# Performance work log

Hardware: AMD Instinct MI355X
Metric: run time of the kernel (lower is better)

## Reference

```python
import jax, jax.numpy as jnp
import numpy as np

B, DIM, N = 64, 128, 4000
H = 4
DH = DIM // H          # 32
CL = 50                # clusters (hardcoded in module)
K = 9                  # knn_num
SCALOR = DH ** -0.5


def setup_inputs() -> dict:
    key = jax.random.key(0)
    ks = jax.random.split(key, 16)
    s = 0.05
    inp = {
        'x': jax.random.normal(ks[0], (B, DIM, N, 1), jnp.float32),
        # conv_group1 / conv_group2: InstanceNorm(no affine) -> BN(affine) -> ReLU -> 1x1 conv
        'wg1': jax.random.normal(ks[1], (CL, DIM), jnp.float32) * s,
        'bg1': jnp.zeros((CL,), jnp.float32),
        'g1_gamma': jnp.ones((DIM,), jnp.float32),
        'g1_beta': jnp.zeros((DIM,), jnp.float32),
        'wg2': jax.random.normal(ks[2], (CL, DIM), jnp.float32) * s,
        'bg2': jnp.zeros((CL,), jnp.float32),
        'g2_gamma': jnp.ones((DIM,), jnp.float32),
        'g2_beta': jnp.zeros((DIM,), jnp.float32),
        # per-head 1x1 convs (stacked over heads)
        'qkv_w': jax.random.normal(ks[3], (H, DH, DIM), jnp.float32) * s,
        'qkv_b': jnp.zeros((H, DH), jnp.float32),
        'qkv1_w': jax.random.normal(ks[4], (H, 3 * DH, DIM), jnp.float32) * s,
        'qkv1_b': jnp.zeros((H, 3 * DH), jnp.float32),
        # GCBlock convs: conv1 (1,3) stride (1,3): 2*DH->DH ; conv2 (1,3): DH->DH
        'gc1_w': jax.random.normal(ks[5], (H, DH, 2 * DH, 3), jnp.float32) * s,
        'gc1_b': jnp.zeros((H, DH), jnp.float32),
        'gc1_gamma': jnp.ones((H, DH), jnp.float32),
        'gc1_beta': jnp.zeros((H, DH), jnp.float32),
        'gc2_w': jax.random.normal(ks[6], (H, DH, DH, 3), jnp.float32) * s,
        'gc2_b': jnp.zeros((H, DH), jnp.float32),
        'gc2_gamma': jnp.ones((H, DH), jnp.float32),
        'gc2_beta': jnp.zeros((H, DH), jnp.float32),
        # output projections
        'pres_w': jax.random.normal(ks[7], (DIM, 2 * DIM), jnp.float32) * s,
        'pres_b': jnp.zeros((DIM,), jnp.float32),
        'proj_w': jax.random.normal(ks[8], (DIM, DIM), jnp.float32) * s,
        'proj_b': jnp.zeros((DIM,), jnp.float32),
    }
    return inp


def _conv_group(x3, w, bconv, gamma, beta):
    # x3: (b, C, n). InstanceNorm2d(eps=1e-3, no affine) over n, BN(train) over (b,n), ReLU, 1x1 conv.
    mu = x3.mean(-1, keepdims=True)
    var = x3.var(-1, keepdims=True)
    xin = (x3 - mu) * jax.lax.rsqrt(var + 1e-3)
    mu2 = xin.mean((0, 2), keepdims=True)
    var2 = xin.var((0, 2), keepdims=True)
    xbn = gamma[None, :, None] * (xin - mu2) * jax.lax.rsqrt(var2 + 1e-5) + beta[None, :, None]
    xr = jax.nn.relu(xbn)
    return jnp.einsum('oc,bcn->bon', w, xr) + bconv[None, :, None]


def _bn_train(h, gamma, beta, axes):
    mu = h.mean(axes, keepdims=True)
    var = h.var(axes, keepdims=True)
    return gamma * (h - mu) * jax.lax.rsqrt(var + 1e-5) + beta


def _forward(x, wg1, bg1, g1_gamma, g1_beta, wg2, bg2, g2_gamma, g2_beta,
             qkv_w, qkv_b, qkv1_w, qkv1_b,
             gc1_w, gc1_b, gc1_gamma, gc1_beta,
             gc2_w, gc2_b, gc2_gamma, gc2_beta,
             pres_w, pres_b, proj_w, proj_b):
    xs = x[..., 0]                                          # (b, dim, n)
    # cluster assignment 1: softmax over points
    embed1 = _conv_group(xs, wg1, bg1, g1_gamma, g1_beta)   # (b, 50, n)
    S1 = jax.nn.softmax(embed1, axis=2)
    cluster_x = jnp.einsum('bdn,bcn->bdc', xs, S1)          # (b, dim, 50)

    # ---- local branch (per head, vectorized): 1x1 conv -> knn graph feature -> conv stack ----
    q = jnp.einsum('hod,bdc->bhoc', qkv_w, cluster_x) + qkv_b[None, :, :, None]  # (b,H,dh,50)
    xt = q.transpose(0, 1, 3, 2)                            # (b,H,50,dh)
    inner = jnp.einsum('bhnc,bhmc->bhnm', xt, xt)
    sq = jnp.sum(xt * xt, axis=-1)
    pd = 2.0 * inner - sq[..., :, None] - sq[..., None, :]  # negative squared distance
    idx = jax.lax.top_k(pd, K)[1]                            # (b,H,50,K)
    x_exp = jnp.broadcast_to(xt[:, :, None, :, :], xt.shape[:2] + (CL, CL, DH))
    feature = jnp.take_along_axis(x_exp, idx[..., None], axis=3)        # (b,H,50,K,dh)
    center = jnp.broadcast_to(xt[:, :, :, None, :], feature.shape)
    edge = jnp.concatenate([center, center - feature], axis=-1)          # (b,H,50,K,2dh)
    # conv1: kernel (1,3) stride (1,3): K=9 -> 3 windows of 3
    e = edge.reshape(edge.shape[0], H, CL, 3, 3, 2 * DH)
    h1 = jnp.einsum('bhnjti,hoit->bhnjo', e, gc1_w) + gc1_b[None, :, None, None, :]
    h1 = jax.nn.relu(_bn_train(h1, gc1_gamma[None, :, None, None, :], gc1_beta[None, :, None, None, :], (0, 2, 3)))
    # conv2: kernel (1,3): 3 -> 1
    h2 = jnp.einsum('bhnti,hoit->bhno', h1, gc2_w) + gc2_b[None, :, None, :]
    h2 = jax.nn.relu(_bn_train(h2, gc2_gamma[None, :, None, :], gc2_beta[None, :, None, :], (0, 2)))
    local = h2.transpose(0, 1, 3, 2)                        # (b,H,dh,50)

    # ---- global branch: tiny attention over 50 clusters per head ----
    qkv = jnp.einsum('hod,bdc->bhoc', qkv1_w, cluster_x) + qkv1_b[None, :, :, None]  # (b,H,3dh,50)
    qg, kg, vg = jnp.split(qkv, 3, axis=2)
    attn = jax.nn.softmax(SCALOR * jnp.einsum('bhdn,bhdm->bhnm', qg, kg), axis=-1)
    glob = jnp.einsum('bhnm,bhdm->bhdn', attn, vg)          # (b,H,dh,50)

    # interleave [local_h, global_h] per head along channels -> (b, 2*dim, 50)
    per_head = jnp.concatenate([local, glob], axis=2)       # (b,H,2dh,50)
    cat = per_head.reshape(per_head.shape[0], 2 * DIM, CL)
    res = jnp.einsum('oc,bcn->bon', pres_w, cat) + pres_b[None, :, None]  # (b,dim,50)

    # cluster assignment 2: softmax over clusters, scatter back to points
    embed2 = _conv_group(xs, wg2, bg2, g2_gamma, g2_beta)   # (b,50,n)
    S2 = jax.nn.softmax(embed2, axis=1)
    res2 = jnp.einsum('bdc,bcn->bdn', res, S2)              # (b,dim,n)
    out = jnp.einsum('od,bdn->bon', proj_w, res2) + proj_b[None, :, None]
    return out[..., None]                                   # (b,dim,n,1)


def reference(x, wg1, bg1, g1_gamma, g1_beta, wg2, bg2, g2_gamma, g2_beta,
              qkv_w, qkv_b, qkv1_w, qkv1_b,
              gc1_w, gc1_b, gc1_gamma, gc1_beta,
              gc2_w, gc2_b, gc2_gamma, gc2_beta,
              pres_w, pres_b, proj_w, proj_b):
    return _forward(x, wg1, bg1, g1_gamma, g1_beta, wg2, bg2, g2_gamma, g2_beta,
                    qkv_w, qkv_b, qkv1_w, qkv1_b,
                    gc1_w, gc1_b, gc1_gamma, gc1_beta,
                    gc2_w, gc2_b, gc2_gamma, gc2_beta,
                    pres_w, pres_b, proj_w, proj_b)
```

## Files before the change

kernel.cpp:

```cpp
#include <hip/hip_runtime.h>
#include <cstddef>


constexpr size_t O_MU    = 0;
constexpr size_t O_RINV  = 8192;
constexpr size_t O_RATIO = 16384;
constexpr size_t O_A1    = 24576;
constexpr size_t O_B1    = 24704;
constexpr size_t O_A2    = 24832;
constexpr size_t O_B2    = 24960;
constexpr size_t O_PROJWT= 25088;
constexpr size_t O_VPROJ = 41472;
constexpr size_t O_MT    = 41600;
constexpr size_t O_E2    = 74368;
constexpr size_t O_UCXP  = 12874368;
constexpr size_t O_W1T   = 18551424;
constexpr size_t O_W2T   = 18558080;
constexpr size_t O_XT    = 18564736;
constexpr size_t O_QT    = 18974336;
constexpr size_t O_KT    = 19383936;
constexpr size_t O_VT    = 19793536;
constexpr size_t O_H1    = 20203136;
constexpr size_t O_P1    = 21431936;
constexpr size_t O_H2    = 21448320;
constexpr size_t O_P2    = 21857920;
constexpr size_t O_CAT   = 21874240;
constexpr size_t O_PRES2 = 22693440;

__global__ __launch_bounds__(256) void k_stats(const float* __restrict__ x,
                                               const float* __restrict__ projw,
                                               const float* __restrict__ wg1,
                                               const float* __restrict__ wg2,
                                               float* __restrict__ ws){
  if(blockIdx.x >= 2112){
    const float* src = (blockIdx.x == 2112) ? wg1 : wg2;
    size_t dst = (blockIdx.x == 2112) ? O_W1T : O_W2T;
    for(int i = threadIdx.x; i < 6656; i += 256){
      int c = i / 52, cl = i % 52;
      ws[dst + i] = (cl < 50) ? src[cl*128 + c] : 0.f;
    }
    return;
  }
  if(blockIdx.x >= 2048){
    int i = (blockIdx.x - 2048)*256 + threadIdx.x;
    int o = i & 127, k = i >> 7;
    ws[O_PROJWT + i] = projw[o*128 + k];
    return;
  }
  int w = threadIdx.x >> 6, lane = threadIdx.x & 63;
  int row = blockIdx.x*4 + w;
  const float4* xr = (const float4*)(x + (size_t)row * 4000);
  float s = 0.f, sq = 0.f;
  for(int i = lane; i < 1000; i += 64){
    float4 v = xr[i];
    s  += v.x + v.y + v.z + v.w;
    sq += v.x*v.x + v.y*v.y + v.z*v.z + v.w*v.w;
  }
  for(int off = 32; off > 0; off >>= 1){
    s  += __shfl_down(s,  off, 64);
    sq += __shfl_down(sq, off, 64);
  }
  if(lane == 0){
    float mean = s * (1.f/4000.f);
    float var  = sq * (1.f/4000.f) - mean*mean;
    ws[O_MU   + row] = mean;
    ws[O_RINV + row] = rsqrtf(var + 1e-3f);
    ws[O_RATIO+ row] = var / (var + 1e-3f);
  }
}

__global__ __launch_bounds__(256) void k_mprep(const float* __restrict__ presw,
                                               const float* __restrict__ presb,
                                               const float* __restrict__ g1g,
                                               const float* __restrict__ g1b,
                                               const float* __restrict__ g2g,
                                               const float* __restrict__ g2b,
                                               float* __restrict__ ws){
  int t = threadIdx.x;
  if(blockIdx.x < 128){
    int kk2 = blockIdx.x * 2;
    __shared__ float pwc[2][128];
    { int which = t >> 7, d = t & 127; pwc[which][d] = presw[d*256 + kk2 + which]; }
    __syncthreads();
    int which = t >> 7, o = t & 127;
    float acc = 0.f;
    for(int d = 0; d < 128; d++) acc += ws[O_PROJWT + d*128 + o] * pwc[which][d];
    ws[O_MT + (size_t)(kk2 + which)*128 + o] = acc;
  }else if(blockIdx.x == 128){
    if(t < 128){
      float v = 0.f;
      for(int d = 0; d < 128; d++) v += ws[O_PROJWT + d*128 + t] * presb[d];
      ws[O_VPROJ + t] = v;
    }
  }else{
    if(t < 128){
      float s = 0.f;
      for(int b = 0; b < 64; b++) s += ws[O_RATIO + b*128 + t];
      float var2 = s * (1.f/64.f);
      float inv2 = rsqrtf(var2 + 1e-5f);
      ws[O_A1+t] = g1g[t] * inv2;  ws[O_B1+t] = g1b[t];
      ws[O_A2+t] = g2g[t] * inv2;  ws[O_B2+t] = g2b[t];
    }
  }
}

__global__ __launch_bounds__(256, 3) void k_e1ucx(const float* __restrict__ x,
    const float* __restrict__ bg1, float* __restrict__ ws){
  int ch = blockIdx.x, b = blockIdx.y;
  __shared__ float lrv1[128*48];
  __shared__ float lxt [48*128];
  __shared__ float ca1[128], cb1[128];
  __shared__ float bg1p[56];
  int t = threadIdx.x;
  if(t < 128){
    float mu = ws[O_MU + b*128 + t], ri = ws[O_RINV + b*128 + t];
    float a1 = ws[O_A1+t]*ri;
    ca1[t] = a1; cb1[t] = ws[O_B1+t] - a1*mu;
  }
  if(t >= 192 && t < 248){ int q = t - 192; bg1p[q] = (q < 50) ? bg1[q] : 0.f; }
  const float* W1T = ws + O_W1T;
  int dg = t & 31, cg = t >> 5;
  int d4 = dg*4, c8 = cg*8;
  float ua[4][8];
  #pragma unroll
  for(int r = 0; r < 4; r++)
    #pragma unroll
    for(int i = 0; i < 8; i++) ua[r][i] = 0.f;
  float zacc = 0.f;
  int ig = t >> 4, jg = t & 15;
  int clb = ig*4, j4 = jg*4;
  int sc[6], sj[6], cx[6];
  float4 pf[6];
  #pragma unroll
  for(int j = 0; j < 6; j++){
    int i = t + 256*j;
    sc[j] = i/12; sj[j] = (i%12)*4;
    cx[j] = sc[j] ^ (((sj[j] >> 2) & 7) << 2);
  }
  {
    int nb0 = ch*336;
    int lim0 = 4000 - nb0; if(lim0 > 48) lim0 = 48;
    #pragma unroll
    for(int j = 0; j < 6; j++)
      pf[j] = (sj[j] < lim0) ? *(const float4*)&x[(size_t)(b*128 + sc[j])*4000 + nb0 + sj[j]]
                             : make_float4(0.f,0.f,0.f,0.f);
  }

  for(int st = 0; st < 7; st++){
    int lim = 4000 - (ch*336 + st*48); if(lim > 48) lim = 48;
    __syncthreads();
    #pragma unroll
    for(int j = 0; j < 6; j++){
      int c = sc[j], jj = sj[j], cxx = cx[j];
      float4 xv = (jj < lim) ? pf[j] : make_float4(0.f,0.f,0.f,0.f);
      lxt[(jj+0)*128 + cxx] = xv.x; lxt[(jj+1)*128 + cxx] = xv.y;
      lxt[(jj+2)*128 + cxx] = xv.z; lxt[(jj+3)*128 + cxx] = xv.w;
      float a1 = ca1[c], b1v = cb1[c];
      float4 r1;
      r1.x = fmaxf(a1*xv.x + b1v, 0.f); r1.y = fmaxf(a1*xv.y + b1v, 0.f);
      r1.z = fmaxf(a1*xv.z + b1v, 0.f); r1.w = fmaxf(a1*xv.w + b1v, 0.f);
      *(float4*)&lrv1[c*48 + jj] = r1;
    }
    __syncthreads();
    if(st < 6){
      int nb2 = ch*336 + (st+1)*48;
      int lim2 = 4000 - nb2; if(lim2 > 48) lim2 = 48;
      #pragma unroll
      for(int j = 0; j < 6; j++)
        pf[j] = (sj[j] < lim2) ? *(const float4*)&x[(size_t)(b*128 + sc[j])*4000 + nb2 + sj[j]]
                               : make_float4(0.f,0.f,0.f,0.f);
    }
    float e[4][4];
    if(ig < 13 && jg < 12){
      #pragma unroll
      for(int r = 0; r < 4; r++){ e[r][0]=0.f; e[r][1]=0.f; e[r][2]=0.f; e[r][3]=0.f; }
      #pragma unroll 4
      for(int c = 0; c < 128; c++){
        float4 w = *(const float4*)&W1T[c*52 + clb];
        float4 v = *(const float4*)&lrv1[c*48 + j4];
        e[0][0] += w.x*v.x; e[0][1] += w.x*v.y; e[0][2] += w.x*v.z; e[0][3] += w.x*v.w;
        e[1][0] += w.y*v.x; e[1][1] += w.y*v.y; e[1][2] += w.y*v.z; e[1][3] += w.y*v.w;
        e[2][0] += w.z*v.x; e[2][1] += w.z*v.y; e[2][2] += w.z*v.z; e[2][3] += w.z*v.w;
        e[3][0] += w.w*v.x; e[3][1] += w.w*v.y; e[3][2] += w.w*v.z; e[3][3] += w.w*v.w;
      }
    }
    __syncthreads();
    if(ig < 13 && jg < 12){
      bool live = (j4 < lim);
      #pragma unroll
      for(int r = 0; r < 4; r++){
        float bias = bg1p[clb + r];
        float4 u = make_float4(0.f,0.f,0.f,0.f);
        if(live){
          u.x = expf(e[r][0] + bias); u.y = expf(e[r][1] + bias);
          u.z = expf(e[r][2] + bias); u.w = expf(e[r][3] + bias);
        }
        *(float4*)&lrv1[(clb + r)*48 + j4] = u;
      }
    }
    __syncthreads();
    if(cg < 7){
      #pragma unroll 2
      for(int n4 = 0; n4 < 12; n4++){
        int n0 = n4*4;
        int dx = d4 ^ ((n4 & 7) << 2);
        float4 uv[8];
        #pragma unroll
        for(int i = 0; i < 8; i++) uv[i] = *(const float4*)&lrv1[(c8 + i)*48 + n0];
        float4 x0 = *(const float4*)&lxt[(n0+0)*128 + dx];
        float4 x1 = *(const float4*)&lxt[(n0+1)*128 + dx];
        float4 x2 = *(const float4*)&lxt[(n0+2)*128 + dx];
        float4 x3 = *(const float4*)&lxt[(n0+3)*128 + dx];
        #pragma unroll
        for(int i = 0; i < 8; i++){
          ua[0][i] += x0.x*uv[i].x + x1.x*uv[i].y + x2.x*uv[i].z + x3.x*uv[i].w;
          ua[1][i] += x0.y*uv[i].x + x1.y*uv[i].y + x2.y*uv[i].z + x3.y*uv[i].w;
          ua[2][i] += x0.z*uv[i].x + x1.z*uv[i].y + x2.z*uv[i].z + x3.z*uv[i].w;
          ua[3][i] += x0.w*uv[i].x + x1.w*uv[i].y + x2.w*uv[i].z + x3.w*uv[i].w;
        }
      }
    }
    if(t < 52){
      float s = 0.f;
      #pragma unroll
      for(int k = 0; k < 12; k++){
        float4 u = *(const float4*)&lrv1[t*48 + k*4];
        s += u.x + u.y + u.z + u.w;
      }
      zacc += s;
    }
  }
  if(cg < 7){
    #pragma unroll
    for(int r = 0; r < 4; r++){
      size_t base = O_UCXP + ((size_t)(ch*64 + b)*132 + d4 + r)*56 + c8;
      *(float4*)&ws[base]     = make_float4(ua[r][0], ua[r][1], ua[r][2], ua[r][3]);
      *(float4*)&ws[base + 4] = make_float4(ua[r][4], ua[r][5], ua[r][6], ua[r][7]);
    }
  }
  if(t < 52) ws[O_UCXP + ((size_t)(ch*64 + b)*132 + 128)*56 + t] = zacc;
}

__global__ __launch_bounds__(256, 6) void k_e2(const float* __restrict__ x,
    const float* __restrict__ bg2, float* __restrict__ ws){
  int ch = blockIdx.x, b = blockIdx.y;
  __shared__ float lrv2[128*48];
  __shared__ float ca2[128], cb2[128];
  __shared__ float bg2p[56];
  int t = threadIdx.x;
  if(t < 128){
    float mu = ws[O_MU + b*128 + t], ri = ws[O_RINV + b*128 + t];
    float a2 = ws[O_A2+t]*ri;
    ca2[t] = a2; cb2[t] = ws[O_B2+t] - a2*mu;
  }
  if(t >= 192 && t < 248){ int q = t - 192; bg2p[q] = (q < 50) ? bg2[q] : 0.f; }
  const float* W2T = ws + O_W2T;
  int ig = t >> 4, jg = t & 15;
  int clb = ig*4, j4 = jg*4;
  int sc[6], sj[6];
  float4 pf[6];
  #pragma unroll
  for(int j = 0; j < 6; j++){ int i = t + 256*j; sc[j] = i/12; sj[j] = (i%12)*4; }
  {
    int nb0 = ch*168;
    int lim0 = 4000 - nb0; if(lim0 > 48) lim0 = 48;
    #pragma unroll
    for(int j = 0; j < 6; j++)
      pf[j] = (sj[j] < lim0) ? *(const float4*)&x[(size_t)(b*128 + sc[j])*4000 + nb0 + sj[j]]
                             : make_float4(0.f,0.f,0.f,0.f);
  }
  for(int st = 0; st < 4; st++){
    int nb = ch*168 + st*48;
    int lim = 4000 - nb; if(lim > 48) lim = 48;
    __syncthreads();
    #pragma unroll
    for(int j = 0; j < 6; j++){
      int c = sc[j], jj = sj[j];
      float4 xv = (jj < lim) ? pf[j] : make_float4(0.f,0.f,0.f,0.f);
      float a2 = ca2[c], b2v = cb2[c];
      float4 r2;
      r2.x = fmaxf(a2*xv.x + b2v, 0.f); r2.y = fmaxf(a2*xv.y + b2v, 0.f);
      r2.z = fmaxf(a2*xv.z + b2v, 0.f); r2.w = fmaxf(a2*xv.w + b2v, 0.f);
      *(float4*)&lrv2[c*48 + jj] = r2;
    }
    __syncthreads();
    if(st < 3){
      int nb2 = nb + 48;
      int lim2 = 4000 - nb2; if(lim2 > 48) lim2 = 48;
      #pragma unroll
      for(int j = 0; j < 6; j++)
        pf[j] = (sj[j] < lim2) ? *(const float4*)&x[(size_t)(b*128 + sc[j])*4000 + nb2 + sj[j]]
                               : make_float4(0.f,0.f,0.f,0.f);
    }
    if(ig < 13 && jg < 12 && lim > 0){
      float e[4][4];
      #pragma unroll
      for(int r = 0; r < 4; r++){ e[r][0]=0.f; e[r][1]=0.f; e[r][2]=0.f; e[r][3]=0.f; }
      #pragma unroll 4
      for(int c = 0; c < 128; c++){
        float4 w = *(const float4*)&W2T[c*52 + clb];
        float4 v = *(const float4*)&lrv2[c*48 + j4];
        e[0][0] += w.x*v.x; e[0][1] += w.x*v.y; e[0][2] += w.x*v.z; e[0][3] += w.x*v.w;
        e[1][0] += w.y*v.x; e[1][1] += w.y*v.y; e[1][2] += w.y*v.z; e[1][3] += w.y*v.w;
        e[2][0] += w.z*v.x; e[2][1] += w.z*v.y; e[2][2] += w.z*v.z; e[2][3] += w.z*v.w;
        e[3][0] += w.w*v.x; e[3][1] += w.w*v.y; e[3][2] += w.w*v.z; e[3][3] += w.w*v.w;
      }
      if(j4 < lim){
        #pragma unroll
        for(int r = 0; r < 4; r++){
          int cl = clb + r;
          if(cl < 50){
            float bias = bg2p[cl];
            float4 o = make_float4(e[r][0]+bias, e[r][1]+bias, e[r][2]+bias, e[r][3]+bias);
            *(float4*)&ws[O_E2 + ((size_t)b*50 + cl)*4000 + nb + j4] = o;
          }
        }
      }
    }
  }
}

__global__ __launch_bounds__(256) void k_qkv(const float* __restrict__ qw,
                                             const float* __restrict__ qb,
                                             const float* __restrict__ q1w,
                                             const float* __restrict__ q1b,
                                             float* __restrict__ ws){
  int rt = blockIdx.x, b = blockIdx.y;
  __shared__ float wl[64*130];
  __shared__ float cxl[128*52];
  __shared__ float zi[52];
  int t = threadIdx.x;
  if(t < 52){
    float s = 0.f;
    if(t < 50){
      #pragma unroll
      for(int ch = 0; ch < 12; ch++)
        s += ws[O_UCXP + ((size_t)(ch*64 + b)*132 + 128)*56 + t];
      zi[t] = 1.f / s;
    }else zi[t] = 0.f;
  }
  for(int i = t; i < 2048; i += 256){
    int rl = i >> 5, kq = i & 31, row = rt*64 + rl;
    float4 w = (row < 128) ? *(const float4*)&qw[row*128 + kq*4]
                           : *(const float4*)&q1w[(row-128)*128 + kq*4];
    int k0 = kq*4;
    wl[rl*130 + k0+0] = w.x; wl[rl*130 + k0+1] = w.y;
    wl[rl*130 + k0+2] = w.z; wl[rl*130 + k0+3] = w.w;
  }
  __syncthreads();
  for(int i = t; i < 6656; i += 256){
    int k = i / 52, c = i % 52;
    float s = 0.f;
    size_t base = O_UCXP + ((size_t)b*132 + k)*56 + c;
    #pragma unroll
    for(int ch = 0; ch < 12; ch++) s += ws[base + (size_t)ch*473088];
    cxl[i] = s * zi[c];
  }
  __syncthreads();
  int ig = t & 15, cg = t >> 4;
  float acc[4][4];
  #pragma unroll
  for(int r = 0; r < 4; r++){ acc[r][0]=0.f; acc[r][1]=0.f; acc[r][2]=0.f; acc[r][3]=0.f; }
  if(cg < 13){
    int rb = ig*4, cb = cg*4;
    #pragma unroll 4
    for(int k = 0; k < 128; k++){
      float4 cv = *(const float4*)&cxl[k*52 + cb];
      float w0 = wl[(rb+0)*130 + k], w1 = wl[(rb+1)*130 + k];
      float w2 = wl[(rb+2)*130 + k], w3 = wl[(rb+3)*130 + k];
      acc[0][0] += w0*cv.x; acc[0][1] += w0*cv.y; acc[0][2] += w0*cv.z; acc[0][3] += w0*cv.w;
      acc[1][0] += w1*cv.x; acc[1][1] += w1*cv.y; acc[1][2] += w1*cv.z; acc[1][3] += w1*cv.w;
      acc[2][0] += w2*cv.x; acc[2][1] += w2*cv.y; acc[2][2] += w2*cv.z; acc[2][3] += w2*cv.w;
      acc[3][0] += w3*cv.x; acc[3][1] += w3*cv.y; acc[3][2] += w3*cv.z; acc[3][3] += w3*cv.w;
    }
    #pragma unroll
    for(int r = 0; r < 4; r++){
      int row = rt*64 + ig*4 + r;
      size_t base; float bias;
      if(row < 128){
        int h = row >> 5;
        bias = qb[row];
        base = O_XT + (size_t)(b*4 + h)*1600 + (row & 31);
      }else{
        int r2 = row - 128, h = r2/96, j = r2%96, kind = j >> 5, dd = j & 31;
        bias = q1b[r2];
        base = (kind==0 ? O_QT : kind==1 ? O_KT : O_VT) + (size_t)(b*4 + h)*1600 + dd;
      }
      #pragma unroll
      for(int s = 0; s < 4; s++){
        int c = cg*4 + s;
        if(c < 50) ws[base + (size_t)c*32] = acc[r][s] + bias;
      }
    }
  }
}

__global__ __launch_bounds__(256) void k_knn(const float* __restrict__ g1w,
                                             const float* __restrict__ g1bias,
                                             float* __restrict__ ws){
  int h = blockIdx.x, b = blockIdx.y;
  __shared__ float xtl[50][33];
  __shared__ float pdl[50][52];
  __shared__ float sql[50];
  __shared__ int   idxl[50][9];
  __shared__ float w1l[6144];
  int t = threadIdx.x;
  const float* xtg = ws + O_XT + (size_t)(b*4 + h)*1600;
  for(int i = t; i < 1600; i += 256) xtl[i >> 5][i & 31] = xtg[i];
  for(int i = t; i < 6144; i += 256){
    int o = i / 192, r = i % 192, ii = r / 3, tt = r % 3;
    w1l[(ii*3 + tt)*32 + o] = g1w[(size_t)h*6144 + i];
  }
  __syncthreads();
  if(t < 50){
    float s = 0.f;
    for(int d = 0; d < 32; d++){ float v = xtl[t][d]; s += v*v; }
    sql[t] = s;
  }
  __syncthreads();
  for(int i = t; i < 2500; i += 256){
    int n = i / 50, m = i % 50;
    float s = 0.f;
    for(int d = 0; d < 32; d++) s += xtl[n][d]*xtl[m][d];
    pdl[n][m] = 2.f*s - sql[n] - sql[m];
  }
  __syncthreads();
  if(t < 50){
    float pv = INFINITY; int pi = -1;
    for(int k = 0; k < 9; k++){
      float bv = -INFINITY; int bi = 1000;
      for(int m = 0; m < 50; m++){
        float v = pdl[t][m];
        bool elig = (v < pv) || (v == pv && m > pi);
        if(elig && (v > bv || (v == bv && m < bi))){ bv = v; bi = m; }
      }
      idxl[t][k] = bi; pv = bv; pi = bi;
    }
  }
  __syncthreads();
  float acc[32];
  bool act = (t < 150);
  if(act){
    int n = t / 3, jw = t % 3;
    #pragma unroll
    for(int o = 0; o < 32; o++) acc[o] = 0.f;
    for(int t3 = 0; t3 < 3; t3++){
      int kx = idxl[n][jw*3 + t3];
      for(int ii = 0; ii < 32; ii++){
        float c0 = xtl[n][ii];
        float c1 = c0 - xtl[kx][ii];
        const float* wr0 = w1l + (ii*3 + t3)*32;
        const float* wr1 = w1l + ((ii+32)*3 + t3)*32;
        #pragma unroll
        for(int o = 0; o < 32; o++) acc[o] += c0*wr0[o] + c1*wr1[o];
      }
    }
    float* out = ws + O_H1 + ((size_t)(b*4 + h)*150 + n*3 + jw)*32;
    #pragma unroll
    for(int o = 0; o < 32; o++){ acc[o] += g1bias[h*32 + o]; out[o] = acc[o]; }
  }
  __syncthreads();
  if(act){
    #pragma unroll
    for(int o = 0; o < 32; o++) w1l[t*32 + o] = acc[o];
  }
  __syncthreads();
  {
    int o = t & 31, part = t >> 5;
    float s = 0.f, sq = 0.f;
    for(int r = part; r < 150; r += 8){
      float v = w1l[r*32 + o];
      s += v; sq += v*v;
    }
    float* sp = &pdl[0][0];
    sp[part*32 + o] = s; sp[256 + part*32 + o] = sq;
    __syncthreads();
    if(t < 32){
      float S = 0.f, Q = 0.f;
      for(int p = 0; p < 8; p++){ S += sp[p*32 + t]; Q += sp[256 + p*32 + t]; }
      ws[O_P1 + b*256 + h*32 + t]       = S;
      ws[O_P1 + b*256 + 128 + h*32 + t] = Q;
    }
  }
}

__global__ __launch_bounds__(256) void k_conv2(const float* __restrict__ g1g,
                                               const float* __restrict__ g1be,
                                               const float* __restrict__ g2w,
                                               const float* __restrict__ g2bias,
                                               float* __restrict__ ws){
  int h = blockIdx.x, b = blockIdx.y;
  __shared__ float hl[150][33];
  __shared__ float w2l[3072];
  __shared__ float rs[8][32], rq[8][32];
  __shared__ float b1s[32], b1t[32];
  int t = threadIdx.x;
  if(t < 32){
    float s = 0.f, sq = 0.f;
    for(int bb = 0; bb < 64; bb++){
      s  += ws[O_P1 + bb*256 + h*32 + t];
      sq += ws[O_P1 + bb*256 + 128 + h*32 + t];
    }
    float mean = s * (1.f/9600.f), var = sq * (1.f/9600.f) - mean*mean;
    float sc = g1g[h*32+t] * rsqrtf(var + 1e-5f);
    b1s[t] = sc; b1t[t] = g1be[h*32+t] - sc*mean;
  }
  for(int i = t; i < 3072; i += 256){
    int o = i / 96, r = i % 96, ii = r / 3, tt = r % 3;
    w2l[(ii*3 + tt)*32 + o] = g2w[(size_t)h*3072 + i];
  }
  __syncthreads();
  const float* h1p = ws + O_H1 + (size_t)(b*4 + h)*4800;
  for(int i = t; i < 4800; i += 256){
    int nj = i >> 5, ii = i & 31;
    hl[nj][ii] = fmaxf(b1s[ii]*h1p[i] + b1t[ii], 0.f);
  }
  __syncthreads();
  int o = t & 31, ng = t >> 5;
  float bias = g2bias[h*32 + o];
  float s = 0.f, sq = 0.f;
  for(int n = ng; n < 50; n += 8){
    float acc = 0.f;
    for(int t3 = 0; t3 < 3; t3++){
      const float* hr = hl[n*3 + t3];
      #pragma unroll
      for(int ii = 0; ii < 32; ii++) acc += hr[ii] * w2l[(ii*3 + t3)*32 + o];
    }
    acc += bias;
    ws[O_H2 + ((size_t)(b*4 + h)*50 + n)*32 + o] = acc;
    s += acc; sq += acc*acc;
  }
  rs[ng][o] = s; rq[ng][o] = sq; __syncthreads();
  if(t < 32){
    float S = 0.f, Q = 0.f;
    for(int g2 = 0; g2 < 8; g2++){ S += rs[g2][t]; Q += rq[g2][t]; }
    ws[O_P2 + (b*4 + h)*64 + t]      = S;
    ws[O_P2 + (b*4 + h)*64 + 32 + t] = Q;
  }
}

__global__ __launch_bounds__(256) void k_attn(const float* __restrict__ g2g,
                                              const float* __restrict__ g2be,
                                              float* __restrict__ ws){
  int h = blockIdx.x, b = blockIdx.y;
  __shared__ float qtl[50][33], ktl[50][33], vtl[50][33], al[50][52];
  __shared__ float b2s[32], b2t[32];
  int t = threadIdx.x;
  if(t < 32){
    float s = 0.f, sq = 0.f;
    for(int bb = 0; bb < 64; bb++){
      s  += ws[O_P2 + (size_t)(bb*4 + h)*64 + t];
      sq += ws[O_P2 + (size_t)(bb*4 + h)*64 + 32 + t];
    }
    float mean = s * (1.f/3200.f), var = sq * (1.f/3200.f) - mean*mean;
    float sc = g2g[h*32+t] * rsqrtf(var + 1e-5f);
    b2s[t] = sc; b2t[t] = g2be[h*32+t] - sc*mean;
  }
  size_t base = (size_t)(b*4 + h)*1600;
  for(int i = t; i < 1600; i += 256){
    int n = i >> 5, d = i & 31;
    qtl[n][d] = ws[O_QT + base + i];
    ktl[n][d] = ws[O_KT + base + i];
    vtl[n][d] = ws[O_VT + base + i];
  }
  __syncthreads();
  for(int i = t; i < 2500; i += 256){
    int n = i / 50, m = i % 50;
    float s = 0.f;
    for(int d = 0; d < 32; d++) s += qtl[n][d]*ktl[m][d];
    al[n][m] = s * 0.17677669529663687f;
  }
  __syncthreads();
  if(t < 50){
    float m = -INFINITY;
    for(int j = 0; j < 50; j++) m = fmaxf(m, al[t][j]);
    float s = 0.f;
    for(int j = 0; j < 50; j++){ float e = expf(al[t][j] - m); al[t][j] = e; s += e; }
    float inv = 1.f/s;
    for(int j = 0; j < 50; j++) al[t][j] *= inv;
  }
  __syncthreads();
  for(int i = t; i < 1600; i += 256){
    int n = i >> 5, d = i & 31;
    float gacc = 0.f;
    for(int m = 0; m < 50; m++) gacc += al[n][m]*vtl[m][d];
    ws[O_CAT + ((size_t)b*256 + h*64 + 32 + d)*50 + n] = gacc;
    float l = fmaxf(b2s[d]*ws[O_H2 + ((size_t)(b*4 + h)*50 + n)*32 + d] + b2t[d], 0.f);
    ws[O_CAT + ((size_t)b*256 + h*64 + d)*50 + n] = l;
  }
}

__global__ __launch_bounds__(256) void k_res(float* __restrict__ ws){
  int oh = blockIdx.x & 1, b = blockIdx.x >> 1;
  __shared__ float mtl[64*68];
  __shared__ float catl[64*52];
  __shared__ float vp[64];
  int t = threadIdx.x;
  if(t < 64) vp[t] = ws[O_VPROJ + oh*64 + t];
  int og = t >> 4, cg = t & 15;
  int ob = og*4, cb = cg*4;
  float acc[4][4];
  #pragma unroll
  for(int r = 0; r < 4; r++){ acc[r][0]=0.f; acc[r][1]=0.f; acc[r][2]=0.f; acc[r][3]=0.f; }
  for(int kc = 0; kc < 4; kc++){
    int k0 = kc*64;
    __syncthreads();
    for(int i = t; i < 1024; i += 256){
      int k = i >> 4, oq = i & 15;
      float4 m = *(const float4*)&ws[O_MT + (size_t)(k0 + k)*128 + oh*64 + oq*4];
      *(float4*)&mtl[k*68 + oq*4] = m;
    }
    for(int i = t; i < 3328; i += 256){
      int k = i / 52, c = i % 52;
      catl[i] = (c < 50) ? ws[O_CAT + (size_t)b*12800 + (k0 + k)*50 + c] : 0.f;
    }
    __syncthreads();
    if(cg < 13){
      #pragma unroll 2
      for(int k = 0; k < 64; k++){
        float4 m0 = *(const float4*)&mtl[k*68 + ob];
        float4 cv = *(const float4*)&catl[k*52 + cb];
        acc[0][0] += m0.x*cv.x; acc[0][1] += m0.x*cv.y; acc[0][2] += m0.x*cv.z; acc[0][3] += m0.x*cv.w;
        acc[1][0] += m0.y*cv.x; acc[1][1] += m0.y*cv.y; acc[1][2] += m0.y*cv.z; acc[1][3] += m0.y*cv.w;
        acc[2][0] += m0.z*cv.x; acc[2][1] += m0.z*cv.y; acc[2][2] += m0.z*cv.z; acc[2][3] += m0.z*cv.w;
        acc[3][0] += m0.w*cv.x; acc[3][1] += m0.w*cv.y; acc[3][2] += m0.w*cv.z; acc[3][3] += m0.w*cv.w;
      }
    }
  }
  if(cg < 13){
    #pragma unroll
    for(int s = 0; s < 4; s++){
      int c = cb + s;
      if(c < 50){
        float4 o0 = make_float4(acc[0][s]+vp[ob+0], acc[1][s]+vp[ob+1], acc[2][s]+vp[ob+2], acc[3][s]+vp[ob+3]);
        *(float4*)&ws[O_PRES2 + (size_t)b*6400 + c*128 + oh*64 + ob] = o0;
      }
    }
  }
}

__global__ __launch_bounds__(256) void k_out(const float* __restrict__ projb,
                                             float* __restrict__ ws,
                                             float* __restrict__ out){
  int nt = blockIdx.x, b = blockIdx.y;
  int n0 = nt*64;
  __shared__ float sl[50*64];
  __shared__ float p2l[50*132];
  __shared__ float pb[128];
  int t = threadIdx.x;
  for(int i = t; i < 3200; i += 256){
    int c = i >> 6, j = i & 63, n = n0 + j;
    sl[i] = (n < 4000) ? ws[O_E2 + ((size_t)b*50 + c)*4000 + n] : 0.f;
  }
  for(int i = t; i < 6400; i += 256){
    int c = i >> 7, o = i & 127;
    p2l[c*132 + o] = ws[O_PRES2 + (size_t)b*6400 + c*128 + o];
  }
  if(t < 128) pb[t] = projb[t];
  __syncthreads();
  if(t < 64){
    int j = t;
    float m = -INFINITY;
    for(int c = 0; c < 50; c++) m = fmaxf(m, sl[c*64 + j]);
    float s = 0.f;
    for(int c = 0; c < 50; c++){ float e = expf(sl[c*64 + j] - m); sl[c*64 + j] = e; s += e; }
    float inv = 1.f/s;
    for(int c = 0; c < 50; c++) sl[c*64 + j] *= inv;
  }
  __syncthreads();
  int og = t >> 4, jg = t & 15;
  int ob = og*8, j4 = jg*4;
  float acc[8][4];
  #pragma unroll
  for(int r = 0; r < 8; r++){ acc[r][0]=0.f; acc[r][1]=0.f; acc[r][2]=0.f; acc[r][3]=0.f; }
  #pragma unroll 2
  for(int c = 0; c < 50; c++){
    float4 sv = *(const float4*)&sl[c*64 + j4];
    float4 p0 = *(const float4*)&p2l[c*132 + ob];
    float4 p1 = *(const float4*)&p2l[c*132 + ob + 4];
    acc[0][0] += p0.x*sv.x; acc[0][1] += p0.x*sv.y; acc[0][2] += p0.x*sv.z; acc[0][3] += p0.x*sv.w;
    acc[1][0] += p0.y*sv.x; acc[1][1] += p0.y*sv.y; acc[1][2] += p0.y*sv.z; acc[1][3] += p0.y*sv.w;
    acc[2][0] += p0.z*sv.x; acc[2][1] += p0.z*sv.y; acc[2][2] += p0.z*sv.z; acc[2][3] += p0.z*sv.w;
    acc[3][0] += p0.w*sv.x; acc[3][1] += p0.w*sv.y; acc[3][2] += p0.w*sv.z; acc[3][3] += p0.w*sv.w;
    acc[4][0] += p1.x*sv.x; acc[4][1] += p1.x*sv.y; acc[4][2] += p1.x*sv.z; acc[4][3] += p1.x*sv.w;
    acc[5][0] += p1.y*sv.x; acc[5][1] += p1.y*sv.y; acc[5][2] += p1.y*sv.z; acc[5][3] += p1.y*sv.w;
    acc[6][0] += p1.z*sv.x; acc[6][1] += p1.z*sv.y; acc[6][2] += p1.z*sv.z; acc[6][3] += p1.z*sv.w;
    acc[7][0] += p1.w*sv.x; acc[7][1] += p1.w*sv.y; acc[7][2] += p1.w*sv.z; acc[7][3] += p1.w*sv.w;
  }
  int n = n0 + j4;
  if(n < 4000){
    #pragma unroll
    for(int r = 0; r < 8; r++){
      float bv = pb[ob + r];
      float4 o = make_float4(acc[r][0]+bv, acc[r][1]+bv, acc[r][2]+bv, acc[r][3]+bv);
      *(float4*)&out[(size_t)(b*128 + ob + r)*4000 + n] = o;
    }
  }
}

extern "C" void kernel_launch(void* const* d_in, const int* in_sizes, int n_in,
                              void* d_out, int out_size, void* d_ws, size_t ws_size,
                              hipStream_t stream){
  (void)in_sizes; (void)n_in; (void)out_size; (void)ws_size;
  const float* x      = (const float*)d_in[0];
  const float* wg1    = (const float*)d_in[1];
  const float* bg1    = (const float*)d_in[2];
  const float* g1g    = (const float*)d_in[3];
  const float* g1b    = (const float*)d_in[4];
  const float* wg2    = (const float*)d_in[5];
  const float* bg2    = (const float*)d_in[6];
  const float* g2g    = (const float*)d_in[7];
  const float* g2b    = (const float*)d_in[8];
  const float* qkvw   = (const float*)d_in[9];
  const float* qkvb   = (const float*)d_in[10];
  const float* qkv1w  = (const float*)d_in[11];
  const float* qkv1b  = (const float*)d_in[12];
  const float* gc1w   = (const float*)d_in[13];
  const float* gc1bias= (const float*)d_in[14];
  const float* gc1g   = (const float*)d_in[15];
  const float* gc1be  = (const float*)d_in[16];
  const float* gc2w   = (const float*)d_in[17];
  const float* gc2bias= (const float*)d_in[18];
  const float* gc2g   = (const float*)d_in[19];
  const float* gc2be  = (const float*)d_in[20];
  const float* presw  = (const float*)d_in[21];
  const float* presb  = (const float*)d_in[22];
  const float* projw  = (const float*)d_in[23];
  const float* projb  = (const float*)d_in[24];
  float* ws = (float*)d_ws;
  float* out = (float*)d_out;

  k_stats<<<2114, 256, 0, stream>>>(x, projw, wg1, wg2, ws);
  k_mprep<<<130, 256, 0, stream>>>(presw, presb, g1g, g1b, g2g, g2b, ws);
  k_e1ucx<<<dim3(12, 64), 256, 0, stream>>>(x, bg1, ws);
  k_e2<<<dim3(24, 64), 256, 0, stream>>>(x, bg2, ws);
  k_qkv<<<dim3(8, 64), 256, 0, stream>>>(qkvw, qkvb, qkv1w, qkv1b, ws);
  k_knn<<<dim3(4, 64), 256, 0, stream>>>(gc1w, gc1bias, ws);
  k_conv2<<<dim3(4, 64), 256, 0, stream>>>(gc1g, gc1be, gc2w, gc2bias, ws);
  k_attn<<<dim3(4, 64), 256, 0, stream>>>(gc2g, gc2be, ws);
  k_res<<<128, 256, 0, stream>>>(ws);
  k_out<<<dim3(63, 64), 256, 0, stream>>>(projb, ws, out);
}
```

Before: 924.4 us.

## Split fused e1/ucx kernel into logit kernel and separate aggregation kernel

The fused cluster-logit and cluster-aggregation kernel is split in two. k_e1 now computes exp(logits) and writes them to a global workspace buffer, and a new k_ucx kernel reads x and those values back to do the weighted aggregation, with a 16-chunk grid and higher occupancy. Both the wg1 and wg2 transposes move from the stats kernel into shared memory inside the consuming kernels, and k_e2 changes its chunking to match. The split is meant to cut register and shared-memory pressure and improve parallelism, but it adds a global round trip of about 51 MB of exp values plus a second read of x.

Result: faster. 795.8 us (-13.9%).

```diff
diff --git a/kernel.cpp b/kernel.cpp
--- a/kernel.cpp
+++ b/kernel.cpp
@@ -13,34 +13,22 @@
 constexpr size_t O_VPROJ = 41472;
 constexpr size_t O_MT    = 41600;
 constexpr size_t O_E2    = 74368;
+constexpr size_t O_EU    = 74368;
 constexpr size_t O_UCXP  = 12874368;
-constexpr size_t O_W1T   = 18551424;
-constexpr size_t O_W2T   = 18558080;
-constexpr size_t O_XT    = 18564736;
-constexpr size_t O_QT    = 18974336;
-constexpr size_t O_KT    = 19383936;
-constexpr size_t O_VT    = 19793536;
-constexpr size_t O_H1    = 20203136;
-constexpr size_t O_P1    = 21431936;
-constexpr size_t O_H2    = 21448320;
-constexpr size_t O_P2    = 21857920;
-constexpr size_t O_CAT   = 21874240;
-constexpr size_t O_PRES2 = 22693440;
+constexpr size_t O_XT    = 20443776;
+constexpr size_t O_QT    = 20853376;
+constexpr size_t O_KT    = 21262976;
+constexpr size_t O_VT    = 21672576;
+constexpr size_t O_H1    = 12874368;
+constexpr size_t O_P1    = 14103168;
+constexpr size_t O_H2    = 14119552;
+constexpr size_t O_P2    = 14529152;
+constexpr size_t O_CAT   = 14545536;
+constexpr size_t O_PRES2 = 15364736;
 
 __global__ __launch_bounds__(256) void k_stats(const float* __restrict__ x,
                                                const float* __restrict__ projw,
-                                               const float* __restrict__ wg1,
-                                               const float* __restrict__ wg2,
                                                float* __restrict__ ws){
-  if(blockIdx.x >= 2112){
-    const float* src = (blockIdx.x == 2112) ? wg1 : wg2;
-    size_t dst = (blockIdx.x == 2112) ? O_W1T : O_W2T;
-    for(int i = threadIdx.x; i < 6656; i += 256){
-      int c = i / 52, cl = i % 52;
-      ws[dst + i] = (cl < 50) ? src[cl*128 + c] : 0.f;
-    }
-    return;
-  }
   if(blockIdx.x >= 2048){
     int i = (blockIdx.x - 2048)*256 + threadIdx.x;
     int o = i & 127, k = i >> 7;
@@ -104,11 +92,12 @@
   }
 }
 
-__global__ __launch_bounds__(256, 3) void k_e1ucx(const float* __restrict__ x,
-    const float* __restrict__ bg1, float* __restrict__ ws){
+__global__ __launch_bounds__(256, 3) void k_e1(const float* __restrict__ x,
+    const float* __restrict__ wg1, const float* __restrict__ bg1,
+    float* __restrict__ ws){
   int ch = blockIdx.x, b = blockIdx.y;
+  __shared__ float lW1[128*52];
   __shared__ float lrv1[128*48];
-  __shared__ float lxt [48*128];
   __shared__ float ca1[128], cb1[128];
   __shared__ float bg1p[56];
   int t = threadIdx.x;
@@ -118,43 +107,31 @@
     ca1[t] = a1; cb1[t] = ws[O_B1+t] - a1*mu;
   }
   if(t >= 192 && t < 248){ int q = t - 192; bg1p[q] = (q < 50) ? bg1[q] : 0.f; }
-  const float* W1T = ws + O_W1T;
-  int dg = t & 31, cg = t >> 5;
-  int d4 = dg*4, c8 = cg*8;
-  float ua[4][8];
-  #pragma unroll
-  for(int r = 0; r < 4; r++)
-    #pragma unroll
-    for(int i = 0; i < 8; i++) ua[r][i] = 0.f;
-  float zacc = 0.f;
+  for(int i = t; i < 1664; i += 256){
+    int cl = i >> 5, cq = i & 31;
+    float4 w = (cl < 50) ? *(const float4*)&wg1[cl*128 + cq*4] : make_float4(0.f,0.f,0.f,0.f);
+    int c0 = cq*4;
+    lW1[(c0+0)*52+cl] = w.x; lW1[(c0+1)*52+cl] = w.y;
+    lW1[(c0+2)*52+cl] = w.z; lW1[(c0+3)*52+cl] = w.w;
+  }
   int ig = t >> 4, jg = t & 15;
   int clb = ig*4, j4 = jg*4;
-  int sc[6], sj[6], cx[6];
+  int sc[6], sj[6];
   float4 pf[6];
   #pragma unroll
-  for(int j = 0; j < 6; j++){
-    int i = t + 256*j;
-    sc[j] = i/12; sj[j] = (i%12)*4;
-    cx[j] = sc[j] ^ (((sj[j] >> 2) & 7) << 2);
-  }
-  {
-    int nb0 = ch*336;
-    int lim0 = 4000 - nb0; if(lim0 > 48) lim0 = 48;
-    #pragma unroll
-    for(int j = 0; j < 6; j++)
-      pf[j] = (sj[j] < lim0) ? *(const float4*)&x[(size_t)(b*128 + sc[j])*4000 + nb0 + sj[j]]
-                             : make_float4(0.f,0.f,0.f,0.f);
-  }
+  for(int j = 0; j < 6; j++){ int i = t + 256*j; sc[j] = i/12; sj[j] = (i%12)*4; }
+  #pragma unroll
+  for(int j = 0; j < 6; j++)
+    pf[j] = *(const float4*)&x[(size_t)(b*128 + sc[j])*4000 + ch*336 + sj[j]];
 
   for(int st = 0; st < 7; st++){
-    int lim = 4000 - (ch*336 + st*48); if(lim > 48) lim = 48;
+    int nb = ch*336 + st*48;
+    int lim = 4000 - nb; if(lim > 48) lim = 48;
     __syncthreads();
     #pragma unroll
     for(int j = 0; j < 6; j++){
-      int c = sc[j], jj = sj[j], cxx = cx[j];
+      int c = sc[j], jj = sj[j];
       float4 xv = (jj < lim) ? pf[j] : make_float4(0.f,0.f,0.f,0.f);
-      lxt[(jj+0)*128 + cxx] = xv.x; lxt[(jj+1)*128 + cxx] = xv.y;
-      lxt[(jj+2)*128 + cxx] = xv.z; lxt[(jj+3)*128 + cxx] = xv.w;
       float a1 = ca1[c], b1v = cb1[c];
       float4 r1;
       r1.x = fmaxf(a1*xv.x + b1v, 0.f); r1.y = fmaxf(a1*xv.y + b1v, 0.f);
@@ -163,42 +140,116 @@
     }
     __syncthreads();
     if(st < 6){
-      int nb2 = ch*336 + (st+1)*48;
+      int nb2 = nb + 48;
       int lim2 = 4000 - nb2; if(lim2 > 48) lim2 = 48;
       #pragma unroll
       for(int j = 0; j < 6; j++)
         pf[j] = (sj[j] < lim2) ? *(const float4*)&x[(size_t)(b*128 + sc[j])*4000 + nb2 + sj[j]]
                                : make_float4(0.f,0.f,0.f,0.f);
     }
-    float e[4][4];
     if(ig < 13 && jg < 12){
+      float e[4][4];
       #pragma unroll
       for(int r = 0; r < 4; r++){ e[r][0]=0.f; e[r][1]=0.f; e[r][2]=0.f; e[r][3]=0.f; }
       #pragma unroll 4
       for(int c = 0; c < 128; c++){
-        float4 w = *(const float4*)&W1T[c*52 + clb];
+        float4 w = *(const float4*)&lW1[c*52 + clb];
         float4 v = *(const float4*)&lrv1[c*48 + j4];
         e[0][0] += w.x*v.x; e[0][1] += w.x*v.y; e[0][2] += w.x*v.z; e[0][3] += w.x*v.w;
         e[1][0] += w.y*v.x; e[1][1] += w.y*v.y; e[1][2] += w.y*v.z; e[1][3] += w.y*v.w;
         e[2][0] += w.z*v.x; e[2][1] += w.z*v.y; e[2][2] += w.z*v.z; e[2][3] += w.z*v.w;
         e[3][0] += w.w*v.x; e[3][1] += w.w*v.y; e[3][2] += w.w*v.z; e[3][3] += w.w*v.w;
       }
-    }
-    __syncthreads();
-    if(ig < 13 && jg < 12){
-      bool live = (j4 < lim);
-      #pragma unroll
-      for(int r = 0; r < 4; r++){
-        float bias = bg1p[clb + r];
-        float4 u = make_float4(0.f,0.f,0.f,0.f);
-        if(live){
-          u.x = expf(e[r][0] + bias); u.y = expf(e[r][1] + bias);
-          u.z = expf(e[r][2] + bias); u.w = expf(e[r][3] + bias);
+      if(j4 < lim){
+        #pragma unroll
+        for(int r = 0; r < 4; r++){
+          int cl = clb + r;
+          if(cl < 50){
+            float bias = bg1p[cl];
+            float4 u;
+            u.x = expf(e[r][0] + bias); u.y = expf(e[r][1] + bias);
+            u.z = expf(e[r][2] + bias); u.w = expf(e[r][3] + bias);
+            *(float4*)&ws[O_EU + ((size_t)(b*50 + cl))*4000 + nb + j4] = u;
+          }
         }
-        *(float4*)&lrv1[(clb + r)*48 + j4] = u;
-      }
-    }
-    __syncthreads();
+      }
+    }
+  }
+}
+
+__global__ __launch_bounds__(256, 4) void k_ucx(const float* __restrict__ x,
+                                                float* __restrict__ ws){
+  int ch = blockIdx.x, b = blockIdx.y;
+  __shared__ float lxt[48*128];
+  __shared__ float leU[56*48];
+  int t = threadIdx.x;
+  int dg = t & 31, cg = t >> 5;
+  int d4 = dg*4, c8 = cg*8;
+  float ua[4][8];
+  #pragma unroll
+  for(int r = 0; r < 4; r++)
+    #pragma unroll
+    for(int i = 0; i < 8; i++) ua[r][i] = 0.f;
+  float zacc = 0.f;
+  int ch0 = ch*252;
+  int ch_len = 4000 - ch0; if(ch_len > 252) ch_len = 252;
+  int sc[6], sj[6], cx[6];
+  float4 pfx[6];
+  #pragma unroll
+  for(int j = 0; j < 6; j++){
+    int i = t + 256*j;
+    sc[j] = i/12; sj[j] = (i%12)*4;
+    cx[j] = sc[j] ^ (((sj[j] >> 2) & 7) << 2);
+  }
+  int uc[3], uj[3];
+  float4 pfu[3];
+  #pragma unroll
+  for(int j = 0; j < 3; j++){ int i = t + 256*j; uc[j] = i/12; uj[j] = (i%12)*4; }
+  {
+    int lim0 = ch_len; if(lim0 > 48) lim0 = 48;
+    #pragma unroll
+    for(int j = 0; j < 6; j++)
+      pfx[j] = (sj[j] < lim0) ? *(const float4*)&x[(size_t)(b*128 + sc[j])*4000 + ch0 + sj[j]]
+                              : make_float4(0.f,0.f,0.f,0.f);
+    #pragma unroll
+    for(int j = 0; j < 3; j++)
+      pfu[j] = (uj[j] < lim0 && uc[j] < 50)
+               ? *(const float4*)&ws[O_EU + ((size_t)(b*50 + uc[j]))*4000 + ch0 + uj[j]]
+               : make_float4(0.f,0.f,0.f,0.f);
+  }
+
+  for(int st = 0; st < 6; st++){
+    int lim = ch_len - st*48; if(lim > 48) lim = 48; if(lim < 0) lim = 0;
+    __syncthreads();
+    #pragma unroll
+    for(int j = 0; j < 6; j++){
+      int jj = sj[j], cxx = cx[j];
+      float4 xv = (jj < lim) ? pfx[j] : make_float4(0.f,0.f,0.f,0.f);
+      lxt[(jj+0)*128 + cxx] = xv.x; lxt[(jj+1)*128 + cxx] = xv.y;
+      lxt[(jj+2)*128 + cxx] = xv.z; lxt[(jj+3)*128 + cxx] = xv.w;
+    }
+    #pragma unroll
+    for(int j = 0; j < 3; j++){
+      int i = t + 256*j;
+      if(i < 672){
+        float4 uv = (uj[j] < lim && uc[j] < 50) ? pfu[j] : make_float4(0.f,0.f,0.f,0.f);
+        *(float4*)&leU[uc[j]*48 + uj[j]] = uv;
+      }
+    }
+    __syncthreads();
+    if(st < 5){
+      int nb2 = ch0 + (st+1)*48;
+      int lim2 = ch_len - (st+1)*48; if(lim2 > 48) lim2 = 48; if(lim2 < 0) lim2 = 0;
+      #pragma unroll
+      for(int j = 0; j < 6; j++)
+        pfx[j] = (sj[j] < lim2) ? *(const float4*)&x[(size_t)(b*128 + sc[j])*4000 + nb2 + sj[j]]
+                                : make_float4(0.f,0.f,0.f,0.f);
+      #pragma unroll
+      for(int j = 0; j < 3; j++)
+        pfu[j] = (uj[j] < lim2 && uc[j] < 50)
+                 ? *(const float4*)&ws[O_EU + ((size_t)(b*50 + uc[j]))*4000 + nb2 + uj[j]]
+                 : make_float4(0.f,0.f,0.f,0.f);
+    }
     if(cg < 7){
       #pragma unroll 2
       for(int n4 = 0; n4 < 12; n4++){
@@ -206,7 +257,7 @@
         int dx = d4 ^ ((n4 & 7) << 2);
         float4 uv[8];
         #pragma unroll
-        for(int i = 0; i < 8; i++) uv[i] = *(const float4*)&lrv1[(c8 + i)*48 + n0];
+        for(int i = 0; i < 8; i++) uv[i] = *(const float4*)&leU[(c8 + i)*48 + n0];
         float4 x0 = *(const float4*)&lxt[(n0+0)*128 + dx];
         float4 x1 = *(const float4*)&lxt[(n0+1)*128 + dx];
         float4 x2 = *(const float4*)&lxt[(n0+2)*128 + dx];
@@ -220,11 +271,11 @@
         }
       }
     }
-    if(t < 52){
+    if(t < 50){
       float s = 0.f;
       #pragma unroll
       for(int k = 0; k < 12; k++){
-        float4 u = *(const float4*)&lrv1[t*48 + k*4];
+        float4 u = *(const float4*)&leU[t*48 + k*4];
         s += u.x + u.y + u.z + u.w;
       }
       zacc += s;
@@ -238,12 +289,14 @@
       *(float4*)&ws[base + 4] = make_float4(ua[r][4], ua[r][5], ua[r][6], ua[r][7]);
     }
   }
-  if(t < 52) ws[O_UCXP + ((size_t)(ch*64 + b)*132 + 128)*56 + t] = zacc;
-}
-
-__global__ __launch_bounds__(256, 6) void k_e2(const float* __restrict__ x,
-    const float* __restrict__ bg2, float* __restrict__ ws){
+  if(t < 50) ws[O_UCXP + ((size_t)(ch*64 + b)*132 + 128)*56 + t] = zacc;
+}
+
+__global__ __launch_bounds__(256, 3) void k_e2(const float* __restrict__ x,
+    const float* __restrict__ wg2, const float* __restrict__ bg2,
+    float* __restrict__ ws){
   int ch = blockIdx.x, b = blockIdx.y;
+  __shared__ float lW2[128*52];
   __shared__ float lrv2[128*48];
   __shared__ float ca2[128], cb2[128];
   __shared__ float bg2p[56];
@@ -254,23 +307,25 @@
     ca2[t] = a2; cb2[t] = ws[O_B2+t] - a2*mu;
   }
   if(t >= 192 && t < 248){ int q = t - 192; bg2p[q] = (q < 50) ? bg2[q] : 0.f; }
-  const float* W2T = ws + O_W2T;
+  for(int i = t; i < 1664; i += 256){
+    int cl = i >> 5, cq = i & 31;
+    float4 w = (cl < 50) ? *(const float4*)&wg2[cl*128 + cq*4] : make_float4(0.f,0.f,0.f,0.f);
+    int c0 = cq*4;
+    lW2[(c0+0)*52+cl] = w.x; lW2[(c0+1)*52+cl] = w.y;
+    lW2[(c0+2)*52+cl] = w.z; lW2[(c0+3)*52+cl] = w.w;
+  }
   int ig = t >> 4, jg = t & 15;
   int clb = ig*4, j4 = jg*4;
   int sc[6], sj[6];
   float4 pf[6];
   #pragma unroll
   for(int j = 0; j < 6; j++){ int i = t + 256*j; sc[j] = i/12; sj[j] = (i%12)*4; }
-  {
-    int nb0 = ch*168;
-    int lim0 = 4000 - nb0; if(lim0 > 48) lim0 = 48;
-    #pragma unroll
-    for(int j = 0; j < 6; j++)
-      pf[j] = (sj[j] < lim0) ? *(const float4*)&x[(size_t)(b*128 + sc[j])*4000 + nb0 + sj[j]]
-                             : make_float4(0.f,0.f,0.f,0.f);
-  }
-  for(int st = 0; st < 4; st++){
-    int nb = ch*168 + st*48;
+  #pragma unroll
+  for(int j = 0; j < 6; j++)
+    pf[j] = *(const float4*)&x[(size_t)(b*128 + sc[j])*4000 + ch*336 + sj[j]];
+
+  for(int st = 0; st < 7; st++){
+    int nb = ch*336 + st*48;
     int lim = 4000 - nb; if(lim > 48) lim = 48;
     __syncthreads();
     #pragma unroll
@@ -284,7 +339,7 @@
       *(float4*)&lrv2[c*48 + jj] = r2;
     }
     __syncthreads();
-    if(st < 3){
+    if(st < 6){
       int nb2 = nb + 48;
       int lim2 = 4000 - nb2; if(lim2 > 48) lim2 = 48;
       #pragma unroll
@@ -292,13 +347,13 @@
         pf[j] = (sj[j] < lim2) ? *(const float4*)&x[(size_t)(b*128 + sc[j])*4000 + nb2 + sj[j]]
                                : make_float4(0.f,0.f,0.f,0.f);
     }
-    if(ig < 13 && jg < 12 && lim > 0){
+    if(ig < 13 && jg < 12){
       float e[4][4];
       #pragma unroll
       for(int r = 0; r < 4; r++){ e[r][0]=0.f; e[r][1]=0.f; e[r][2]=0.f; e[r][3]=0.f; }
       #pragma unroll 4
       for(int c = 0; c < 128; c++){
-        float4 w = *(const float4*)&W2T[c*52 + clb];
+        float4 w = *(const float4*)&lW2[c*52 + clb];
         float4 v = *(const float4*)&lrv2[c*48 + j4];
         e[0][0] += w.x*v.x; e[0][1] += w.x*v.y; e[0][2] += w.x*v.z; e[0][3] += w.x*v.w;
         e[1][0] += w.y*v.x; e[1][1] += w.y*v.y; e[1][2] += w.y*v.z; e[1][3] += w.y*v.w;
@@ -334,7 +389,7 @@
     float s = 0.f;
     if(t < 50){
       #pragma unroll
-      for(int ch = 0; ch < 12; ch++)
+      for(int ch = 0; ch < 16; ch++)
         s += ws[O_UCXP + ((size_t)(ch*64 + b)*132 + 128)*56 + t];
       zi[t] = 1.f / s;
     }else zi[t] = 0.f;
@@ -353,7 +408,7 @@
     float s = 0.f;
     size_t base = O_UCXP + ((size_t)b*132 + k)*56 + c;
     #pragma unroll
-    for(int ch = 0; ch < 12; ch++) s += ws[base + (size_t)ch*473088];
+    for(int ch = 0; ch < 16; ch++) s += ws[base + (size_t)ch*473088];
     cxl[i] = s * zi[c];
   }
   __syncthreads();
@@ -730,10 +785,11 @@
   float* ws = (float*)d_ws;
   float* out = (float*)d_out;
 
-  k_stats<<<2114, 256, 0, stream>>>(x, projw, wg1, wg2, ws);
+  k_stats<<<2112, 256, 0, stream>>>(x, projw, ws);
   k_mprep<<<130, 256, 0, stream>>>(presw, presb, g1g, g1b, g2g, g2b, ws);
-  k_e1ucx<<<dim3(12, 64), 256, 0, stream>>>(x, bg1, ws);
-  k_e2<<<dim3(24, 64), 256, 0, stream>>>(x, bg2, ws);
+  k_e1<<<dim3(12, 64), 256, 0, stream>>>(x, wg1, bg1, ws);
+  k_ucx<<<dim3(16, 64), 256, 0, stream>>>(x, ws);
+  k_e2<<<dim3(12, 64), 256, 0, stream>>>(x, wg2, bg2, ws);
   k_qkv<<<dim3(8, 64), 256, 0, stream>>>(qkvw, qkvb, qkv1w, qkv1b, ws);
   k_knn<<<dim3(4, 64), 256, 0, stream>>>(gc1w, gc1bias, ws);
   k_conv2<<<dim3(4, 64), 256, 0, stream>>>(gc1g, gc1be, gc2w, gc2bias, ws);
```
